# Performance work log

Measured on AMD Instinct MI355X. Metric: run time of the kernel, lower is better.

## Reference

```python
import jax, jax.numpy as jnp
import numpy as np

EMBED_DIM = 2048
NUM_Q_HEADS = 16
NUM_KV_HEADS = 4
HEAD_DIM = EMBED_DIM // NUM_Q_HEADS  # 128
N_REP = NUM_Q_HEADS // NUM_KV_HEADS  # 4


def setup_inputs() -> dict:
    key = jax.random.key(0)
    ks = jax.random.split(key, 8)
    B, T, C = 2, 2048, EMBED_DIM
    s = 0.02
    return {
        "x": jax.random.normal(ks[0], (B, T, C), dtype=jnp.float32),
        "Wq": jax.random.normal(ks[1], (C, NUM_Q_HEADS * HEAD_DIM), dtype=jnp.float32) * s,
        "bq": jax.random.normal(ks[2], (NUM_Q_HEADS * HEAD_DIM,), dtype=jnp.float32) * s,
        "Wk": jax.random.normal(ks[3], (C, NUM_KV_HEADS * HEAD_DIM), dtype=jnp.float32) * s,
        "bk": jax.random.normal(ks[4], (NUM_KV_HEADS * HEAD_DIM,), dtype=jnp.float32) * s,
        "Wv": jax.random.normal(ks[5], (C, NUM_KV_HEADS * HEAD_DIM), dtype=jnp.float32) * s,
        "bv": jax.random.normal(ks[6], (NUM_KV_HEADS * HEAD_DIM,), dtype=jnp.float32) * s,
        "Wo": jax.random.normal(ks[7], (C, C), dtype=jnp.float32) * s,
    }


def reference(x, Wq, bq, Wk, bk, Wv, bv, Wo):
    B, T, C = x.shape
    # Projections (torch Linear with bias; weights stored as [in, out])
    q = (x @ Wq + bq).reshape(B, T, NUM_KV_HEADS, N_REP, HEAD_DIM)
    k = (x @ Wk + bk).reshape(B, T, NUM_KV_HEADS, HEAD_DIM)
    v = (x @ Wv + bv).reshape(B, T, NUM_KV_HEADS, HEAD_DIM)
    # GQA: group query heads per kv head instead of materializing repeated K/V.
    # q: [B, G, n_rep, Tq, d], k/v: [B, G, Tk, d]
    q = q.transpose(0, 2, 3, 1, 4)  # B, G, n_rep, T, d
    k = k.transpose(0, 2, 1, 3)     # B, G, T, d
    v = v.transpose(0, 2, 1, 3)
    scale = 1.0 / jnp.sqrt(jnp.asarray(HEAD_DIM, dtype=x.dtype))
    scores = jnp.einsum('bgnqd,bgkd->bgnqk', q, k) * scale
    attn = jax.nn.softmax(scores, axis=-1)
    out = jnp.einsum('bgnqk,bgkd->bgnqd', attn, v)  # B, G, n_rep, T, d
    # merge heads back: (G, n_rep) -> Hq, then [B, T, C]
    out = out.transpose(0, 3, 1, 2, 4).reshape(B, T, C)
    return out @ Wo
```

## Files before the change

kernel.cpp:

```cpp
#include <hip/hip_runtime.h>
#include <hip/hip_bf16.h>
#include <cstdint>
#include <cstddef>

typedef __bf16 bf16;
typedef __attribute__((ext_vector_type(8))) __bf16 bf16x8;
typedef __attribute__((ext_vector_type(4))) float f32x4;
typedef __attribute__((ext_vector_type(16))) float f32x16;

#define KPAD 136
#define VPAD 72

__device__ __forceinline__ void async16(const void* g, void* l) {
  __builtin_amdgcn_global_load_lds(
      (const __attribute__((address_space(1))) void*)g,
      (__attribute__((address_space(3))) void*)l,
      16, 0, 0);
}

__global__ void cvt_x(const float* __restrict__ in, bf16* __restrict__ out, int n8) {
  int i = blockIdx.x * 256 + threadIdx.x;
  if (i >= n8) return;
  const float* src = in + (size_t)i * 8;
  float4 f0 = *reinterpret_cast<const float4*>(src);
  float4 f1 = *reinterpret_cast<const float4*>(src + 4);
  bf16x8 v = {(bf16)f0.x, (bf16)f0.y, (bf16)f0.z, (bf16)f0.w,
              (bf16)f1.x, (bf16)f1.y, (bf16)f1.z, (bf16)f1.w};
  *reinterpret_cast<bf16x8*>(out + (size_t)i * 8) = v;
}

template <typename CT, bool HAS_BIAS>
__global__ __launch_bounds__(256, 2)
void gemm_bt(const bf16* __restrict__ A, const bf16* __restrict__ Bt,
             const bf16* __restrict__ bias, CT* __restrict__ C,
             int M, int N, int K) {
  __shared__ bf16 As[128 * 32];
  __shared__ bf16 Bs[128 * 32];
  const int tid = threadIdx.x;
  const int wave = tid >> 6, lane = tid & 63;
  const int quad = lane >> 4, l15 = lane & 15;
  const int row0 = blockIdx.y * 128;
  const int col0 = blockIdx.x * 128;
  const int wm = wave & 1, wn = wave >> 1;

  const f32x4 fz = {0.f, 0.f, 0.f, 0.f};
  f32x4 acc[4][4];
#pragma unroll
  for (int i = 0; i < 4; ++i)
#pragma unroll
    for (int j = 0; j < 4; ++j) acc[i][j] = fz;

  for (int k0 = 0; k0 < K; k0 += 32) {
    __syncthreads();
#pragma unroll
    for (int j = 0; j < 2; ++j) {
      int c = tid + j * 256;
      int r = c >> 2;
      int kk = (c & 3) * 8;
      async16(A + (size_t)(row0 + r) * K + k0 + kk, &As[c * 8]);
      async16(Bt + (size_t)(col0 + r) * K + k0 + kk, &Bs[c * 8]);
    }
    __syncthreads();

    bf16x8 a[4], b[4];
#pragma unroll
    for (int i = 0; i < 4; ++i)
      a[i] = *reinterpret_cast<const bf16x8*>(&As[(wm * 64 + i * 16 + l15) * 32 + quad * 8]);
#pragma unroll
    for (int j = 0; j < 4; ++j)
      b[j] = *reinterpret_cast<const bf16x8*>(&Bs[(wn * 64 + j * 16 + l15) * 32 + quad * 8]);
#pragma unroll
    for (int i = 0; i < 4; ++i)
#pragma unroll
      for (int j = 0; j < 4; ++j)
        acc[i][j] = __builtin_amdgcn_mfma_f32_16x16x32_bf16(a[i], b[j], acc[i][j], 0, 0, 0);
  }

#pragma unroll
  for (int i = 0; i < 4; ++i) {
    int m = row0 + wm * 64 + i * 16 + quad * 4;
#pragma unroll
    for (int j = 0; j < 4; ++j) {
      int n = col0 + wn * 64 + j * 16 + l15;
      float bv = HAS_BIAS ? (float)bias[n] : 0.f;
#pragma unroll
      for (int r = 0; r < 4; ++r)
        C[(size_t)(m + r) * N + n] = (CT)(acc[i][j][r] + bv);
    }
  }
}

__global__ void transpose2d_cvt(const float* __restrict__ in, bf16* __restrict__ out,
                                int R, int C) {
  __shared__ float t[32][33];
  const int tx = threadIdx.x & 31, ty = threadIdx.x >> 5;
  const int c0 = blockIdx.x * 32, r0 = blockIdx.y * 32;
#pragma unroll
  for (int i = 0; i < 4; ++i)
    t[ty + i * 8][tx] = in[(size_t)(r0 + ty + i * 8) * C + c0 + tx];
  __syncthreads();
#pragma unroll
  for (int i = 0; i < 4; ++i)
    out[(size_t)(c0 + ty + i * 8) * R + r0 + tx] = (bf16)t[tx][ty + i * 8];
}

__global__ void transpose_v(const bf16* __restrict__ QKV, bf16* __restrict__ Vt) {
  const int z = blockIdx.z;
  const int b = z >> 2, g = z & 3;
  const bf16* in = QKV + (size_t)b * 2048 * 3072 + 2560 + g * 128;
  bf16* out = Vt + (size_t)z * 128 * 2048;
  __shared__ bf16 t[32][33];
  const int tx = threadIdx.x & 31, ty = threadIdx.x >> 5;
  const int d0 = blockIdx.x * 32;
  const int t0 = blockIdx.y * 32;
#pragma unroll
  for (int i = 0; i < 4; ++i)
    t[ty + i * 8][tx] = in[(size_t)(t0 + ty + i * 8) * 3072 + d0 + tx];
  __syncthreads();
#pragma unroll
  for (int i = 0; i < 4; ++i)
    out[(size_t)(d0 + ty + i * 8) * 2048 + t0 + tx] = t[tx][ty + i * 8];
}

__global__ void concat_bias(const float* __restrict__ bq, const float* __restrict__ bk,
                            const float* __restrict__ bv, bf16* __restrict__ out) {
  int i = blockIdx.x * 256 + threadIdx.x;
  float v;
  if (i < 2048) v = bq[i];
  else if (i < 2560) v = bk[i - 2048];
  else v = bv[i - 2560];
  out[i] = (bf16)v;
}

__global__ __launch_bounds__(256, 2)
void attn_kernel(const bf16* __restrict__ QKV, const bf16* __restrict__ Vt,
                 bf16* __restrict__ Out) {
  const int bid = blockIdx.x;
  const int qt = bid & 15;
  const int bh = bid >> 4;
  const int b = bh >> 4, h = bh & 15, g = h >> 2;
  const int tid = threadIdx.x;
  const int wave = tid >> 6, lane = tid & 63;
  const int l31 = lane & 31, half = lane >> 5;

  __shared__ bf16 smem[17920];
  bf16* Ks  = smem;
  bf16* Vts = smem + 8704;
  bf16* Qstage = smem;

  const bf16* Qbase = QKV + ((size_t)b * 2048 + qt * 128) * 3072 + h * 128;
#pragma unroll
  for (int j = 0; j < 8; ++j) {
    int c = tid + j * 256;
    *reinterpret_cast<bf16x8*>(&Qstage[(c >> 4) * KPAD + (c & 15) * 8]) =
        *reinterpret_cast<const bf16x8*>(Qbase + (size_t)(c >> 4) * 3072 + (c & 15) * 8);
  }
  __syncthreads();
  bf16x8 qf[8];
#pragma unroll
  for (int ks = 0; ks < 8; ++ks)
    qf[ks] = *reinterpret_cast<const bf16x8*>(
        &Qstage[(wave * 32 + l31) * KPAD + ks * 16 + half * 8]);

  const bf16* Kbase = QKV + (size_t)b * 2048 * 3072 + 2048 + g * 128;
  const bf16* Vbase = Vt + (size_t)(b * 4 + g) * 128 * 2048;

  f32x16 po[4];
#pragma unroll
  for (int j = 0; j < 4; ++j)
#pragma unroll
    for (int r = 0; r < 16; ++r) po[j][r] = 0.f;
  float lsum = 0.f;
  const float sc = 0.08838834764831845f;

  for (int t0 = 0; t0 < 2048; t0 += 64) {
    __syncthreads();
#pragma unroll
    for (int j = 0; j < 4; ++j) {
      int c = tid + j * 256;
      *reinterpret_cast<bf16x8*>(&Ks[(c >> 4) * KPAD + (c & 15) * 8]) =
          *reinterpret_cast<const bf16x8*>(Kbase + (size_t)(t0 + (c >> 4)) * 3072 + (c & 15) * 8);
      *reinterpret_cast<bf16x8*>(&Vts[(c >> 3) * VPAD + (c & 7) * 8]) =
          *reinterpret_cast<const bf16x8*>(Vbase + (size_t)(c >> 3) * 2048 + t0 + (c & 7) * 8);
    }
    __syncthreads();

    f32x16 s[2];
#pragma unroll
    for (int nt = 0; nt < 2; ++nt)
#pragma unroll
      for (int r = 0; r < 16; ++r) s[nt][r] = 0.f;
#pragma unroll
    for (int ks = 0; ks < 8; ++ks) {
#pragma unroll
      for (int nt = 0; nt < 2; ++nt) {
        bf16x8 kf = *reinterpret_cast<const bf16x8*>(
            &Ks[(nt * 32 + l31) * KPAD + ks * 16 + half * 8]);
        s[nt] = __builtin_amdgcn_mfma_f32_32x32x16_bf16(kf, qf[ks], s[nt], 0, 0, 0);
      }
    }

#pragma unroll
    for (int nt = 0; nt < 2; ++nt)
#pragma unroll
      for (int r = 0; r < 16; ++r) {
        float p = __expf(s[nt][r] * sc);
        lsum += p;
        s[nt][r] = p;
      }

#pragma unroll
    for (int ks2 = 0; ks2 < 4; ++ks2) {
      const int nt = ks2 >> 1;
      const int a = (ks2 & 1) * 8;
      uint32_t x0, x1, x2, x3;
      asm("v_cvt_pk_bf16_f32 %0, %1, %2" : "=v"(x0) : "v"(s[nt][a + 0]), "v"(s[nt][a + 1]));
      asm("v_cvt_pk_bf16_f32 %0, %1, %2" : "=v"(x1) : "v"(s[nt][a + 2]), "v"(s[nt][a + 3]));
      asm("v_cvt_pk_bf16_f32 %0, %1, %2" : "=v"(x2) : "v"(s[nt][a + 4]), "v"(s[nt][a + 5]));
      asm("v_cvt_pk_bf16_f32 %0, %1, %2" : "=v"(x3) : "v"(s[nt][a + 6]), "v"(s[nt][a + 7]));
      asm("v_permlane32_swap_b32 %0, %1" : "+v"(x0), "+v"(x2));
      asm("v_permlane32_swap_b32 %0, %1" : "+v"(x1), "+v"(x3));
      union { uint32_t u[4]; bf16x8 v; } pu;
      pu.u[0] = x0; pu.u[1] = x1; pu.u[2] = x2; pu.u[3] = x3;
      const bf16x8 pf = pu.v;
#pragma unroll
      for (int nd = 0; nd < 4; ++nd) {
        bf16x8 vf = *reinterpret_cast<const bf16x8*>(
            &Vts[(nd * 32 + l31) * VPAD + ks2 * 16 + half * 8]);
        po[nd] = __builtin_amdgcn_mfma_f32_32x32x16_bf16(pf, vf, po[nd], 0, 0, 0);
      }
    }
  }

  float l = lsum + __shfl_xor(lsum, 32, 64);
  float inv = 1.0f / l;

  const size_t qrow0 = (size_t)b * 2048 + (size_t)qt * 128 + wave * 32;
#pragma unroll
  for (int r = 0; r < 16; ++r) {
    int row = (r & 3) + 8 * (r >> 2) + 4 * half;
    float invr = __shfl(inv, row, 64);
#pragma unroll
    for (int nt = 0; nt < 4; ++nt)
      Out[(qrow0 + row) * 2048 + h * 128 + nt * 32 + l31] = (bf16)(po[nt][r] * invr);
  }
}

extern "C" void kernel_launch(void* const* d_in, const int* in_sizes, int n_in,
                              void* d_out, int out_size, void* d_ws, size_t ws_size,
                              hipStream_t stream) {
  const float* x  = (const float*)d_in[0];
  const float* Wq = (const float*)d_in[1];
  const float* bq = (const float*)d_in[2];
  const float* Wk = (const float*)d_in[3];
  const float* bk = (const float*)d_in[4];
  const float* Wv = (const float*)d_in[5];
  const float* bv = (const float*)d_in[6];
  const float* Wo = (const float*)d_in[7];
  float* out = (float*)d_out;
  bf16* ws = (bf16*)d_ws;

  bf16* wqkvT = ws;
  bf16* biasq = ws + 6291456;
  bf16* woT   = ws + 6294528;
  bf16* qkv   = ws + 10488832;
  bf16* vt    = ws + 23071744;
  bf16* aout  = ws + 25168896;
  bf16* xb    = ws + 33557504;

  cvt_x<<<4096, 256, 0, stream>>>(x, xb, 1048576);
  transpose2d_cvt<<<dim3(64, 64), 256, 0, stream>>>(Wq, wqkvT, 2048, 2048);
  transpose2d_cvt<<<dim3(16, 64), 256, 0, stream>>>(Wk, wqkvT + 2048 * 2048, 2048, 512);
  transpose2d_cvt<<<dim3(16, 64), 256, 0, stream>>>(Wv, wqkvT + 2560 * 2048, 2048, 512);
  transpose2d_cvt<<<dim3(64, 64), 256, 0, stream>>>(Wo, woT, 2048, 2048);
  concat_bias<<<12, 256, 0, stream>>>(bq, bk, bv, biasq);

  gemm_bt<bf16, true><<<dim3(24, 32), 256, 0, stream>>>(xb, wqkvT, biasq, qkv, 4096, 3072, 2048);

  transpose_v<<<dim3(4, 64, 8), 256, 0, stream>>>(qkv, vt);

  attn_kernel<<<512, 256, 0, stream>>>(qkv, vt, aout);

  gemm_bt<float, false><<<dim3(16, 32), 256, 0, stream>>>(aout, woT, nullptr, out, 4096, 2048, 2048);
}
```

Baseline: 309.8 us.

## Double-buffer GEMM tiles with K=64 steps and XOR-swizzled LDS layout

The projection GEMM now loads 64-wide K tiles into two LDS buffers, prefetching the next tile with async global-to-LDS loads while MFMAs run on the current one. This removes one barrier per iteration, and the XOR swizzle of 16-byte chunks is meant to avoid LDS bank conflicts on fragment reads. In exchange, LDS use grows to 64KB per block, which may limit occupancy below the requested two blocks per CU.

```diff
diff --git a/kernel.cpp b/kernel.cpp
--- a/kernel.cpp
+++ b/kernel.cpp
@@ -34,14 +34,14 @@
 void gemm_bt(const bf16* __restrict__ A, const bf16* __restrict__ Bt,
              const bf16* __restrict__ bias, CT* __restrict__ C,
              int M, int N, int K) {
-  __shared__ bf16 As[128 * 32];
-  __shared__ bf16 Bs[128 * 32];
+  __shared__ bf16 smem[4][128 * 64];
   const int tid = threadIdx.x;
   const int wave = tid >> 6, lane = tid & 63;
   const int quad = lane >> 4, l15 = lane & 15;
   const int row0 = blockIdx.y * 128;
   const int col0 = blockIdx.x * 128;
   const int wm = wave & 1, wn = wave >> 1;
+  const int sw = l15 & 7;
 
   const f32x4 fz = {0.f, 0.f, 0.f, 0.f};
   f32x4 acc[4][4];
@@ -50,31 +50,52 @@
 #pragma unroll
     for (int j = 0; j < 4; ++j) acc[i][j] = fz;
 
-  for (int k0 = 0; k0 < K; k0 += 32) {
+#define STAGE(buf, k0)                                                         \
+  {                                                                            \
+    _Pragma("unroll")                                                          \
+    for (int j = 0; j < 4; ++j) {                                              \
+      int c = tid + j * 256;                                                   \
+      int r = c >> 3;                                                          \
+      int gs = (c & 7) ^ (r & 7);                                              \
+      async16(A + (size_t)(row0 + r) * K + (k0) + gs * 8, &smem[(buf)*2][c * 8]);   \
+      async16(Bt + (size_t)(col0 + r) * K + (k0) + gs * 8, &smem[(buf)*2 + 1][c * 8]); \
+    }                                                                          \
+  }
+
+  STAGE(0, 0);
+  __syncthreads();
+
+  const int nt = K >> 6;
+  for (int t = 0; t < nt; ++t) {
+    const int cur = t & 1;
+    if (t + 1 < nt) STAGE(cur ^ 1, (t + 1) << 6);
+
+    const bf16* As = smem[cur * 2];
+    const bf16* Bs = smem[cur * 2 + 1];
+    bf16x8 a[4][2], b[4][2];
+#pragma unroll
+    for (int mf = 0; mf < 4; ++mf) {
+      int ra = wm * 64 + mf * 16 + l15;
+      int rb = wn * 64 + mf * 16 + l15;
+#pragma unroll
+      for (int ks = 0; ks < 2; ++ks) {
+        int pg = (ks * 4 + quad) ^ sw;
+        a[mf][ks] = *reinterpret_cast<const bf16x8*>(&As[ra * 64 + pg * 8]);
+        b[mf][ks] = *reinterpret_cast<const bf16x8*>(&Bs[rb * 64 + pg * 8]);
+      }
+    }
+#pragma unroll
+    for (int ks = 0; ks < 2; ++ks)
+#pragma unroll
+      for (int mf = 0; mf < 4; ++mf)
+#pragma unroll
+        for (int nf = 0; nf < 4; ++nf)
+          acc[mf][nf] = __builtin_amdgcn_mfma_f32_16x16x32_bf16(a[mf][ks], b[nf][ks],
+                                                                acc[mf][nf], 0, 0, 0);
+
     __syncthreads();
-#pragma unroll
-    for (int j = 0; j < 2; ++j) {
-      int c = tid + j * 256;
-      int r = c >> 2;
-      int kk = (c & 3) * 8;
-      async16(A + (size_t)(row0 + r) * K + k0 + kk, &As[c * 8]);
-      async16(Bt + (size_t)(col0 + r) * K + k0 + kk, &Bs[c * 8]);
-    }
-    __syncthreads();
-
-    bf16x8 a[4], b[4];
-#pragma unroll
-    for (int i = 0; i < 4; ++i)
-      a[i] = *reinterpret_cast<const bf16x8*>(&As[(wm * 64 + i * 16 + l15) * 32 + quad * 8]);
-#pragma unroll
-    for (int j = 0; j < 4; ++j)
-      b[j] = *reinterpret_cast<const bf16x8*>(&Bs[(wn * 64 + j * 16 + l15) * 32 + quad * 8]);
-#pragma unroll
-    for (int i = 0; i < 4; ++i)
-#pragma unroll
-      for (int j = 0; j < 4; ++j)
-        acc[i][j] = __builtin_amdgcn_mfma_f32_16x16x32_bf16(a[i], b[j], acc[i][j], 0, 0, 0);
-  }
+  }
+#undef STAGE
 
 #pragma unroll
   for (int i = 0; i < 4; ++i) {
```

Result: faster. 296.4 us (-4.3%).
